# Kernel tuning notes

Hardware: AMD Instinct MI355X
Metric: run time of the kernel (lower is better)

Reference implementation:

```python
import jax, jax.numpy as jnp
import numpy as np

N, F, H, E = 8192, 512, 128, 262144
EDGE_REMOVE_RATE = 0.3   # forward arg edge_remove_rate
FEATURE_MASK_RATE = 0.2  # forward arg feature_mask_rate
TEMPERATURE = 0.2        # __init__ temperature


def setup_inputs() -> dict:
    key = jax.random.key(0)
    ks = jax.random.split(key, 8)
    x = jax.random.normal(ks[0], (N, F), jnp.float32)
    row = jax.random.randint(ks[1], (E,), 0, N, dtype=jnp.int32)
    col = jax.random.randint(ks[2], (E,), 0, N, dtype=jnp.int32)
    W_enc = jax.random.normal(ks[3], (F, H), jnp.float32) / np.sqrt(F)
    W_edge = jax.random.normal(ks[4], (2 * H, 1), jnp.float32) / np.sqrt(2 * H)
    b_edge = jnp.zeros((1,), jnp.float32)
    # uniform noise for the RelaxedBernoulli reparameterized sample (one per dense entry)
    noise = jax.random.uniform(ks[5], (N, N), jnp.float32, 1e-6, 1.0 - 1e-6)
    # per-feature uniforms for random_drop_feature's column mask
    mask_u = jax.random.uniform(ks[6], (F,), jnp.float32)
    return dict(x=x, row=row, col=col, W_enc=W_enc, W_edge=W_edge,
                b_edge=b_edge, noise=noise, mask_u=mask_u)


def reference(x, row, col, W_enc, W_edge, b_edge, noise, mask_u):
    # random_drop_feature: zero out columns where uniform < drop_prob
    drop = mask_u < FEATURE_MASK_RATE                      # [F] bool
    feature = jnp.where(drop[None, :], 0.0, x)             # [N, F]

    # encoder(x, sp_adj): 1-layer GCN, sparse A @ (x @ W) via segment_sum over edges
    xw = x @ W_enc                                         # [N, H]
    agg = jax.ops.segment_sum(xw[col], row, num_segments=N)  # [N, H]
    node_emb = jax.nn.relu(agg)

    # fc_edge on concat(node_emb[row], node_emb[col]) == split-weight form
    W1, W2 = W_edge[:H], W_edge[H:]                        # [H,1] each
    edge_logits = (node_emb[row] @ W1 + node_emb[col] @ W2 + b_edge).reshape(-1)  # [E]

    # _norm_to_interval(logits, ub=edge_remove_rate, lb=max(rate-0.5, 0))
    ub = EDGE_REMOVE_RATE
    lb = max(EDGE_REMOVE_RATE - 0.5, 0.0)
    lo = edge_logits.min()
    k = (ub - lb) / (edge_logits.max() - lo)
    edge_probs = lb + k * (edge_logits - lo)               # [E]

    remove_prob = jnp.zeros((N, N), jnp.float32).at[row, col].set(edge_probs)
    sp_dense = jnp.zeros((N, N), jnp.float32).at[row, col].set(1.0)

    # RelaxedBernoulliStraightThrough.rsample():
    #   soft = sigmoid((logit(p) + logistic_noise) / temperature); hard = round(soft)
    eps = 1e-10  # keeps logit(0) finite; sigmoid((log eps)/T) == 0 in fp32
    logit_p = jnp.log(remove_prob + eps) - jnp.log1p(-remove_prob + eps)
    logistic = jnp.log(noise) - jnp.log1p(-noise)
    soft = jax.nn.sigmoid((logit_p + logistic) / TEMPERATURE)
    hard = jnp.round(soft)
    remove_adj = hard + soft - jax.lax.stop_gradient(soft)  # straight-through

    # adj = (1 - remove_adj) * to_dense(sp_adj); aug rate = nnz(adj)/nnz(sp_adj)
    adj = (1.0 - remove_adj) * sp_dense                    # [N, N]
    adj_aug_rate = jnp.sum(adj != 0).astype(jnp.float32) / jnp.sum(sp_dense != 0).astype(jnp.float32)
    return feature, adj, adj_aug_rate
```

## Files before the change

kernel.cpp:

```cpp
#include <hip/hip_runtime.h>
#include <math.h>

constexpr int NND = 8192;
constexpr int FD  = 512;
constexpr int HD  = 128;
constexpr int ED  = 262144;
constexpr long long NF_ = (long long)NND * FD;
constexpr long long NN_ = (long long)NND * NND;

constexpr int SLOT = 72;

constexpr long long Z_K1 = 0;
constexpr long long Z_KD = 6291456;
constexpr long long Z_KE = 8388608;
constexpr long long Z_KF = 14680064;

constexpr int GEMMB = 512;
constexpr int SCAT_BASE = GEMMB;
constexpr int FEAT_BASE = GEMMB + 1024;


__global__ void k0_init(int* __restrict__ cnt, unsigned* __restrict__ ctrl) {
    int t = blockIdx.x * 256 + threadIdx.x;
    if (t < NND) cnt[t] = 0;
    if (t < 16) ctrl[t] = 0u;
}

__global__ __launch_bounds__(256) void k1_mega(const float* __restrict__ x,
                                               const float* __restrict__ W,
                                               const float* __restrict__ mask_u,
                                               const int* __restrict__ row,
                                               const int* __restrict__ col,
                                               float* __restrict__ out,
                                               float* __restrict__ xw,
                                               int* __restrict__ cnt,
                                               int* __restrict__ slot) {
    __shared__ float Wt[32 * 128];
    __shared__ float Xt[16][32];
    int tid = threadIdx.x;
    if (blockIdx.x < GEMMB) {
        int bid = blockIdx.x;
        int tx = tid & 31, ty = tid >> 5;
        int m0 = bid * 16;
        int r0 = ty * 2, r1 = r0 + 1;
        float a0[4] = {0.f, 0.f, 0.f, 0.f};
        float a1[4] = {0.f, 0.f, 0.f, 0.f};
        for (int kt = 0; kt < FD; kt += 32) {
            const float4* Wq = (const float4*)(W + (long long)kt * HD);
            float4* Wtq = (float4*)Wt;
#pragma unroll
            for (int j = 0; j < 4; ++j)
                Wtq[tid + j * 256] = Wq[tid + j * 256];
            if (tid < 128) {
                int r = tid >> 3, kq = tid & 7;
                ((float4*)&Xt[r][0])[kq] =
                    *(const float4*)(x + (long long)(m0 + r) * FD + kt + kq * 4);
            }
            __syncthreads();
#pragma unroll 8
            for (int kk = 0; kk < 32; ++kk) {
                float s0 = Xt[r0][kk], s1 = Xt[r1][kk];
                const float4 b = *(const float4*)&Wt[kk * 128 + tx * 4];
                a0[0] = fmaf(s0, b.x, a0[0]);
                a0[1] = fmaf(s0, b.y, a0[1]);
                a0[2] = fmaf(s0, b.z, a0[2]);
                a0[3] = fmaf(s0, b.w, a0[3]);
                a1[0] = fmaf(s1, b.x, a1[0]);
                a1[1] = fmaf(s1, b.y, a1[1]);
                a1[2] = fmaf(s1, b.z, a1[2]);
                a1[3] = fmaf(s1, b.w, a1[3]);
            }
            __syncthreads();
        }
        *(float4*)(xw + (long long)(m0 + r0) * HD + tx * 4) =
            make_float4(a0[0], a0[1], a0[2], a0[3]);
        *(float4*)(xw + (long long)(m0 + r1) * HD + tx * 4) =
            make_float4(a1[0], a1[1], a1[2], a1[3]);
    } else if (blockIdx.x < FEAT_BASE) {
        int e = (blockIdx.x - SCAT_BASE) * 256 + tid;
        int r = row[e];
        int pos = atomicAdd(&cnt[r], 1);
        slot[r * SLOT + pos] = (e << 13) | col[e];
        float4* zq = (float4*)(out + NF_);
        float4 z = make_float4(0.f, 0.f, 0.f, 0.f);
#pragma unroll
        for (int j = 0; j < 8; ++j)
            zq[Z_KD + e + (long long)j * ED] = z;
    } else {
        int fid = (blockIdx.x - FEAT_BASE) * 256 + tid;
        int c4 = (fid & 127) * 4;
        float kx = (mask_u[c4 + 0] < 0.2f) ? 0.f : 1.f;
        float ky = (mask_u[c4 + 1] < 0.2f) ? 0.f : 1.f;
        float kz = (mask_u[c4 + 2] < 0.2f) ? 0.f : 1.f;
        float kw = (mask_u[c4 + 3] < 0.2f) ? 0.f : 1.f;
        const float4* xq = (const float4*)x;
        float4* oq = (float4*)out;
#pragma unroll
        for (int j = 0; j < 4; ++j) {
            long long q = fid + (long long)j * 262144;
            float4 xv = xq[q];
            float4 o;
            o.x = xv.x * kx; o.y = xv.y * ky; o.z = xv.z * kz; o.w = xv.w * kw;
            oq[q] = o;
        }
        float4* zq = (float4*)(out + NF_);
        float4 z = make_float4(0.f, 0.f, 0.f, 0.f);
#pragma unroll
        for (int j = 0; j < 24; ++j)
            zq[Z_K1 + fid + (long long)j * 262144] = z;
    }
}

__global__ __launch_bounds__(128) void kE_spmm_uv(const float* __restrict__ xw,
                                                  const int* __restrict__ cnt,
                                                  const int* __restrict__ slot,
                                                  const float* __restrict__ Wedge,
                                                  float* __restrict__ u,
                                                  float* __restrict__ v,
                                                  float4* __restrict__ zq) {
    int i = blockIdx.x, t = threadIdx.x;
    int n = cnt[i];
    const int* sp = slot + i * SLOT;
    float acc = 0.f;
    int j = 0;
    for (; j + 4 <= n; j += 4) {
        int c0 = sp[j] & 8191, c1 = sp[j + 1] & 8191;
        int c2 = sp[j + 2] & 8191, c3 = sp[j + 3] & 8191;
        float v0 = xw[(long long)c0 * HD + t];
        float v1 = xw[(long long)c1 * HD + t];
        float v2 = xw[(long long)c2 * HD + t];
        float v3 = xw[(long long)c3 * HD + t];
        acc += v0; acc += v1; acc += v2; acc += v3;
    }
    for (; j < n; ++j) acc += xw[(long long)(sp[j] & 8191) * HD + t];
    acc = fmaxf(acc, 0.f);

    float up = acc * Wedge[t];
    float vp = acc * Wedge[HD + t];
#pragma unroll
    for (int off = 32; off > 0; off >>= 1) {
        up += __shfl_down(up, off);
        vp += __shfl_down(vp, off);
    }
    __shared__ float su[2], sv[2];
    int wid = t >> 6;
    if ((t & 63) == 0) { su[wid] = up; sv[wid] = vp; }
    __syncthreads();
    if (t == 0) { u[i] = su[0] + su[1]; v[i] = sv[0] + sv[1]; }

    long long ft = (long long)i * 128 + t;
    float4 z = make_float4(0.f, 0.f, 0.f, 0.f);
#pragma unroll
    for (int jj = 0; jj < 6; ++jj)
        zq[Z_KE + ft + (long long)jj * 1048576] = z;
}

__global__ __launch_bounds__(256) void kF_minmax(const int* __restrict__ row,
                                                 const int* __restrict__ col,
                                                 const float* __restrict__ u,
                                                 const float* __restrict__ v,
                                                 const float* __restrict__ b_edge,
                                                 float* __restrict__ pmn,
                                                 float* __restrict__ pmx,
                                                 unsigned* __restrict__ ctrl,
                                                 float4* __restrict__ zq) {
    int gid = blockIdx.x * 256 + threadIdx.x;
    float el = u[row[gid]] + v[col[gid]] + b_edge[0];

    float4 z = make_float4(0.f, 0.f, 0.f, 0.f);
#pragma unroll
    for (int j = 0; j < 8; ++j)
        zq[Z_KF + gid + (long long)j * ED] = z;

    float mn = el, mx = el;
#pragma unroll
    for (int off = 32; off > 0; off >>= 1) {
        mn = fminf(mn, __shfl_xor(mn, off));
        mx = fmaxf(mx, __shfl_xor(mx, off));
    }
    __shared__ float smn[4], smx[4];
    __shared__ unsigned tkt;
    int w = threadIdx.x >> 6;
    if ((threadIdx.x & 63) == 0) { smn[w] = mn; smx[w] = mx; }
    __syncthreads();
    if (threadIdx.x == 0) {
        pmn[blockIdx.x] = fminf(fminf(smn[0], smn[1]), fminf(smn[2], smn[3]));
        pmx[blockIdx.x] = fmaxf(fmaxf(smx[0], smx[1]), fmaxf(smx[2], smx[3]));
        __threadfence();
        tkt = atomicAdd(&ctrl[4], 1u);
    }
    __syncthreads();
    if (tkt == gridDim.x - 1) {
        __threadfence();
        int t = threadIdx.x;
        float4 a = ((const float4*)pmn)[t];
        float4 b = ((const float4*)pmx)[t];
        float m2 = fminf(fminf(a.x, a.y), fminf(a.z, a.w));
        float x2 = fmaxf(fmaxf(b.x, b.y), fmaxf(b.z, b.w));
#pragma unroll
        for (int off = 32; off > 0; off >>= 1) {
            m2 = fminf(m2, __shfl_xor(m2, off));
            x2 = fmaxf(x2, __shfl_xor(x2, off));
        }
        __shared__ float rmn[4], rmx[4];
        if ((t & 63) == 0) { rmn[t >> 6] = m2; rmx[t >> 6] = x2; }
        __syncthreads();
        if (t == 0) {
            float* flh = (float*)&ctrl[8];
            flh[0] = fminf(fminf(rmn[0], rmn[1]), fminf(rmn[2], rmn[3]));
            flh[1] = fmaxf(fmaxf(rmx[0], rmx[1]), fmaxf(rmx[2], rmx[3]));
        }
    }
}

__global__ __launch_bounds__(256) void kZ_patch(const int* __restrict__ cnt,
                                                const int* __restrict__ slot,
                                                const float* __restrict__ u,
                                                const float* __restrict__ v,
                                                const float* __restrict__ b_edge,
                                                const float* __restrict__ noise,
                                                float* __restrict__ adj,
                                                int* __restrict__ pcu,
                                                int* __restrict__ pcz,
                                                unsigned* __restrict__ ctrl,
                                                float* __restrict__ rate) {
    const int tid = threadIdx.x;
    const int b = blockIdx.x;
    __shared__ int skey[8 * SLOT];
    __shared__ int scnt[8];
    __shared__ float su_[8];
    if (tid < 8) {
        scnt[tid] = cnt[b * 8 + tid];
        su_[tid] = u[b * 8 + tid];
    }
    __syncthreads();
#pragma unroll
    for (int rl = 0; rl < 8; ++rl) {
        int n = scnt[rl];
        for (int i = tid; i < n; i += 256)
            skey[rl * SLOT + i] = slot[(b * 8 + rl) * SLOT + i];
    }
    __syncthreads();

    const float* flh = (const float*)&ctrl[8];
    const float lo = flh[0];
    const float hi = flh[1];
    const float kk = 0.3f / (hi - lo);
    const float be = b_edge[0];

    int uniq = 0, nzc = 0;
#pragma unroll
    for (int rl = 0; rl < 8; ++rl) {
        int n = scnt[rl];
        const int* kp = skey + rl * SLOT;
        for (int i = tid; i < n; i += 256) {
            int key = kp[i];
            int c = key & 8191;
            bool win = true;
            for (int j = 0; j < n; ++j) {
                int kj = kp[j];
                if ((kj & 8191) == c && kj > key) { win = false; break; }
            }
            if (!win) continue;
            ++uniq;
            float el = su_[rl] + v[c] + be;
            float pr = kk * (el - lo);
            float lp = logf(pr + 1e-10f) - log1pf(1e-10f - pr);
            float nz = noise[(long long)(b * 8 + rl) * NND + c];
            float lg = logf(nz) - log1pf(-nz);
            if ((lp + lg) <= 0.f) {
                ++nzc;
                adj[(long long)(b * 8 + rl) * NND + c] = 1.0f;
            }
        }
    }

#pragma unroll
    for (int off = 32; off > 0; off >>= 1) {
        uniq += __shfl_down(uniq, off);
        nzc  += __shfl_down(nzc, off);
    }
    __shared__ int scu[4], scz[4];
    __shared__ unsigned tkt;
    int wd = tid >> 6;
    if ((tid & 63) == 0) { scu[wd] = uniq; scz[wd] = nzc; }
    __syncthreads();
    if (tid == 0) {
        pcu[b] = scu[0] + scu[1] + scu[2] + scu[3];
        pcz[b] = scz[0] + scz[1] + scz[2] + scz[3];
        __threadfence();
        tkt = atomicAdd(&ctrl[5], 1u);
    }
    __syncthreads();
    if (tkt == gridDim.x - 1) {
        __threadfence();
        int t = tid;
        int4 a = ((const int4*)pcu)[t];
        int4 bq = ((const int4*)pcz)[t];
        int cu = a.x + a.y + a.z + a.w;
        int cz = bq.x + bq.y + bq.z + bq.w;
#pragma unroll
        for (int off = 32; off > 0; off >>= 1) {
            cu += __shfl_down(cu, off);
            cz += __shfl_down(cz, off);
        }
        __shared__ int rcu[4], rcz[4];
        if ((t & 63) == 0) { rcu[t >> 6] = cu; rcz[t >> 6] = cz; }
        __syncthreads();
        if (t == 0)
            rate[0] = (float)(rcz[0] + rcz[1] + rcz[2] + rcz[3]) /
                      (float)(rcu[0] + rcu[1] + rcu[2] + rcu[3]);
    }
}

extern "C" void kernel_launch(void* const* d_in, const int* in_sizes, int n_in,
                              void* d_out, int out_size, void* d_ws, size_t ws_size,
                              hipStream_t stream) {
    const float* x     = (const float*)d_in[0];
    const int*   row   = (const int*)d_in[1];
    const int*   col   = (const int*)d_in[2];
    const float* Wenc  = (const float*)d_in[3];
    const float* Wedge = (const float*)d_in[4];
    const float* bedge = (const float*)d_in[5];
    const float* noise = (const float*)d_in[6];
    const float* masku = (const float*)d_in[7];
    float* out = (float*)d_out;

    char* ws = (char*)d_ws;
    float* xw   = (float*)(ws);
    int*   slot = (int*)  (ws + 4194304);
    float* u    = (float*)(ws + 6553600);
    float* v    = (float*)(ws + 6586368);
    int*   cnt  = (int*)  (ws + 6619136);
    int*   pcu  = (int*)  (ws + 6651904);
    int*   pcz  = (int*)  (ws + 6656000);
    float* pmn  = (float*)(ws + 6660096);
    float* pmx  = (float*)(ws + 6664192);
    unsigned* ctrl = (unsigned*)(ws + 6668288);

    float4* zq  = (float4*)(out + NF_);
    float*  adj = out + NF_;
    float* rate = out + NF_ + NN_;

    k0_init<<<32, 256, 0, stream>>>(cnt, ctrl);
    k1_mega<<<GEMMB + 1024 + 1024, 256, 0, stream>>>(x, Wenc, masku, row, col,
                                                     out, xw, cnt, slot);
    kE_spmm_uv<<<8192, 128, 0, stream>>>(xw, cnt, slot, Wedge, u, v, zq);
    kF_minmax<<<1024, 256, 0, stream>>>(row, col, u, v, bedge, pmn, pmx, ctrl, zq);
    kZ_patch<<<1024, 256, 0, stream>>>(cnt, slot, u, v, bedge, noise, adj,
                                       pcu, pcz, ctrl, rate);
}
```

Before: 211.2 us.

## Move dense adjacency zero-fill into a dedicated fill kernel

Takes the 256 MB zero-fill of the dense adjacency output out of the GEMM, scatter, SpMM and min/max kernels and puts it in one standalone streaming fill kernel launched first. The edge-slot scatter is folded into the feature-mask blocks, which shrinks k1_mega's grid. The aim is a simpler pure-bandwidth fill with fewer blocks and better coalescing. In exchange it gives up hiding the fill behind the compute-bound and latency-bound phases, so the fill now runs serially before them.

```diff
diff --git a/kernel.cpp b/kernel.cpp
--- a/kernel.cpp
+++ b/kernel.cpp
@@ -7,23 +7,26 @@
 constexpr int ED  = 262144;
 constexpr long long NF_ = (long long)NND * FD;
 constexpr long long NN_ = (long long)NND * NND;
+constexpr long long NN4 = NN_ / 4;
 
 constexpr int SLOT = 72;
 
-constexpr long long Z_K1 = 0;
-constexpr long long Z_KD = 6291456;
-constexpr long long Z_KE = 8388608;
-constexpr long long Z_KF = 14680064;
-
 constexpr int GEMMB = 512;
-constexpr int SCAT_BASE = GEMMB;
-constexpr int FEAT_BASE = GEMMB + 1024;
+constexpr int FEAT_BASE = GEMMB;
 
 
 __global__ void k0_init(int* __restrict__ cnt, unsigned* __restrict__ ctrl) {
     int t = blockIdx.x * 256 + threadIdx.x;
     if (t < NND) cnt[t] = 0;
     if (t < 16) ctrl[t] = 0u;
+}
+
+__global__ __launch_bounds__(256) void kFill(float4* __restrict__ zq) {
+    int gid = blockIdx.x * 256 + threadIdx.x;
+    float4 z = make_float4(0.f, 0.f, 0.f, 0.f);
+#pragma unroll
+    for (int j = 0; j < 32; ++j)
+        zq[(long long)j * 524288 + gid] = z;
 }
 
 __global__ __launch_bounds__(256) void k1_mega(const float* __restrict__ x,
@@ -76,18 +79,11 @@
             make_float4(a0[0], a0[1], a0[2], a0[3]);
         *(float4*)(xw + (long long)(m0 + r1) * HD + tx * 4) =
             make_float4(a1[0], a1[1], a1[2], a1[3]);
-    } else if (blockIdx.x < FEAT_BASE) {
-        int e = (blockIdx.x - SCAT_BASE) * 256 + tid;
-        int r = row[e];
-        int pos = atomicAdd(&cnt[r], 1);
-        slot[r * SLOT + pos] = (e << 13) | col[e];
-        float4* zq = (float4*)(out + NF_);
-        float4 z = make_float4(0.f, 0.f, 0.f, 0.f);
-#pragma unroll
-        for (int j = 0; j < 8; ++j)
-            zq[Z_KD + e + (long long)j * ED] = z;
     } else {
         int fid = (blockIdx.x - FEAT_BASE) * 256 + tid;
+        int r = row[fid];
+        int pos = atomicAdd(&cnt[r], 1);
+        slot[r * SLOT + pos] = (fid << 13) | col[fid];
         int c4 = (fid & 127) * 4;
         float kx = (mask_u[c4 + 0] < 0.2f) ? 0.f : 1.f;
         float ky = (mask_u[c4 + 1] < 0.2f) ? 0.f : 1.f;
@@ -103,11 +99,6 @@
             o.x = xv.x * kx; o.y = xv.y * ky; o.z = xv.z * kz; o.w = xv.w * kw;
             oq[q] = o;
         }
-        float4* zq = (float4*)(out + NF_);
-        float4 z = make_float4(0.f, 0.f, 0.f, 0.f);
-#pragma unroll
-        for (int j = 0; j < 24; ++j)
-            zq[Z_K1 + fid + (long long)j * 262144] = z;
     }
 }
 
@@ -116,8 +107,7 @@
                                                   const int* __restrict__ slot,
                                                   const float* __restrict__ Wedge,
                                                   float* __restrict__ u,
-                                                  float* __restrict__ v,
-                                                  float4* __restrict__ zq) {
+                                                  float* __restrict__ v) {
     int i = blockIdx.x, t = threadIdx.x;
     int n = cnt[i];
     const int* sp = slot + i * SLOT;
@@ -147,12 +137,6 @@
     if ((t & 63) == 0) { su[wid] = up; sv[wid] = vp; }
     __syncthreads();
     if (t == 0) { u[i] = su[0] + su[1]; v[i] = sv[0] + sv[1]; }
-
-    long long ft = (long long)i * 128 + t;
-    float4 z = make_float4(0.f, 0.f, 0.f, 0.f);
-#pragma unroll
-    for (int jj = 0; jj < 6; ++jj)
-        zq[Z_KE + ft + (long long)jj * 1048576] = z;
 }
 
 __global__ __launch_bounds__(256) void kF_minmax(const int* __restrict__ row,
@@ -162,15 +146,9 @@
                                                  const float* __restrict__ b_edge,
                                                  float* __restrict__ pmn,
                                                  float* __restrict__ pmx,
-                                                 unsigned* __restrict__ ctrl,
-                                                 float4* __restrict__ zq) {
+                                                 unsigned* __restrict__ ctrl) {
     int gid = blockIdx.x * 256 + threadIdx.x;
     float el = u[row[gid]] + v[col[gid]] + b_edge[0];
-
-    float4 z = make_float4(0.f, 0.f, 0.f, 0.f);
-#pragma unroll
-    for (int j = 0; j < 8; ++j)
-        zq[Z_KF + gid + (long long)j * ED] = z;
 
     float mn = el, mx = el;
 #pragma unroll
@@ -343,10 +321,11 @@
     float* rate = out + NF_ + NN_;
 
     k0_init<<<32, 256, 0, stream>>>(cnt, ctrl);
-    k1_mega<<<GEMMB + 1024 + 1024, 256, 0, stream>>>(x, Wenc, masku, row, col,
-                                                     out, xw, cnt, slot);
-    kE_spmm_uv<<<8192, 128, 0, stream>>>(xw, cnt, slot, Wedge, u, v, zq);
-    kF_minmax<<<1024, 256, 0, stream>>>(row, col, u, v, bedge, pmn, pmx, ctrl, zq);
+    kFill<<<2048, 256, 0, stream>>>(zq);
+    k1_mega<<<GEMMB + 1024, 256, 0, stream>>>(x, Wenc, masku, row, col,
+                                              out, xw, cnt, slot);
+    kE_spmm_uv<<<8192, 128, 0, stream>>>(xw, cnt, slot, Wedge, u, v);
+    kF_minmax<<<1024, 256, 0, stream>>>(row, col, u, v, bedge, pmn, pmx, ctrl);
     kZ_patch<<<1024, 256, 0, stream>>>(cnt, slot, u, v, bedge, noise, adj,
                                        pcu, pcz, ctrl, rate);
 }
```

Measured after the change: 221.5 us. 1.05x slower.

## Enlarge GEMM register tile to 4x8 per thread with transposed X tile

Applied to the files above, without the earlier changes.

The x@W_enc GEMM portion of the mega kernel now computes 64 rows per block instead of 16, with each thread holding a 4x8 accumulator tile. The X tile is stored transposed in shared memory so it can be read as float4. This raises arithmetic intensity and cuts shared-memory loads per FMA. In exchange there are 4x fewer GEMM blocks (128), which may underfill the GPU, and register pressure goes up.

```diff
diff --git a/kernel.cpp b/kernel.cpp
--- a/kernel.cpp
+++ b/kernel.cpp
@@ -15,7 +15,7 @@
 constexpr long long Z_KE = 8388608;
 constexpr long long Z_KF = 14680064;
 
-constexpr int GEMMB = 512;
+constexpr int GEMMB = 128;
 constexpr int SCAT_BASE = GEMMB;
 constexpr int FEAT_BASE = GEMMB + 1024;
 
@@ -36,46 +36,57 @@
                                                int* __restrict__ cnt,
                                                int* __restrict__ slot) {
     __shared__ float Wt[32 * 128];
-    __shared__ float Xt[16][32];
+    __shared__ float Xt[32][64];
     int tid = threadIdx.x;
     if (blockIdx.x < GEMMB) {
         int bid = blockIdx.x;
-        int tx = tid & 31, ty = tid >> 5;
-        int m0 = bid * 16;
-        int r0 = ty * 2, r1 = r0 + 1;
-        float a0[4] = {0.f, 0.f, 0.f, 0.f};
-        float a1[4] = {0.f, 0.f, 0.f, 0.f};
+        int tx = tid & 15;
+        int ty = tid >> 4;
+        int m0 = bid * 64;
+        float a[4][8];
+#pragma unroll
+        for (int ri = 0; ri < 4; ++ri)
+#pragma unroll
+            for (int ci = 0; ci < 8; ++ci) a[ri][ci] = 0.f;
+
         for (int kt = 0; kt < FD; kt += 32) {
             const float4* Wq = (const float4*)(W + (long long)kt * HD);
             float4* Wtq = (float4*)Wt;
 #pragma unroll
             for (int j = 0; j < 4; ++j)
                 Wtq[tid + j * 256] = Wq[tid + j * 256];
-            if (tid < 128) {
-                int r = tid >> 3, kq = tid & 7;
-                ((float4*)&Xt[r][0])[kq] =
-                    *(const float4*)(x + (long long)(m0 + r) * FD + kt + kq * 4);
+#pragma unroll
+            for (int j = 0; j < 2; ++j) {
+                int task = tid + j * 256;
+                int r = task >> 3, kq = task & 7;
+                float4 xv = *(const float4*)(x + (long long)(m0 + r) * FD + kt + kq * 4);
+                Xt[kq * 4 + 0][r] = xv.x;
+                Xt[kq * 4 + 1][r] = xv.y;
+                Xt[kq * 4 + 2][r] = xv.z;
+                Xt[kq * 4 + 3][r] = xv.w;
             }
             __syncthreads();
 #pragma unroll 8
             for (int kk = 0; kk < 32; ++kk) {
-                float s0 = Xt[r0][kk], s1 = Xt[r1][kk];
-                const float4 b = *(const float4*)&Wt[kk * 128 + tx * 4];
-                a0[0] = fmaf(s0, b.x, a0[0]);
-                a0[1] = fmaf(s0, b.y, a0[1]);
-                a0[2] = fmaf(s0, b.z, a0[2]);
-                a0[3] = fmaf(s0, b.w, a0[3]);
-                a1[0] = fmaf(s1, b.x, a1[0]);
-                a1[1] = fmaf(s1, b.y, a1[1]);
-                a1[2] = fmaf(s1, b.z, a1[2]);
-                a1[3] = fmaf(s1, b.w, a1[3]);
+                float4 b0 = *(const float4*)&Wt[kk * 128 + tx * 8];
+                float4 b1 = *(const float4*)&Wt[kk * 128 + tx * 8 + 4];
+                float4 xr = *(const float4*)&Xt[kk][ty * 4];
+                float xs[4] = {xr.x, xr.y, xr.z, xr.w};
+                float bs[8] = {b0.x, b0.y, b0.z, b0.w, b1.x, b1.y, b1.z, b1.w};
+#pragma unroll
+                for (int ri = 0; ri < 4; ++ri)
+#pragma unroll
+                    for (int ci = 0; ci < 8; ++ci)
+                        a[ri][ci] = fmaf(xs[ri], bs[ci], a[ri][ci]);
             }
             __syncthreads();
         }
-        *(float4*)(xw + (long long)(m0 + r0) * HD + tx * 4) =
-            make_float4(a0[0], a0[1], a0[2], a0[3]);
-        *(float4*)(xw + (long long)(m0 + r1) * HD + tx * 4) =
-            make_float4(a1[0], a1[1], a1[2], a1[3]);
+#pragma unroll
+        for (int ri = 0; ri < 4; ++ri) {
+            float* orow = xw + (long long)(m0 + ty * 4 + ri) * HD + tx * 8;
+            *(float4*)orow = make_float4(a[ri][0], a[ri][1], a[ri][2], a[ri][3]);
+            *(float4*)(orow + 4) = make_float4(a[ri][4], a[ri][5], a[ri][6], a[ri][7]);
+        }
     } else if (blockIdx.x < FEAT_BASE) {
         int e = (blockIdx.x - SCAT_BASE) * 256 + tid;
         int r = row[e];
```

After: 220.8 us. 4.5% more time.
